# Kernel optimization log

Hardware: AMD Instinct MI355X
Metric: run time of the kernel (lower is better)

The kernel has to match this reference:

```python
import jax, jax.numpy as jnp
import numpy as np

B, N, C, H = 2, 4096, 256, 4
DH = C // H  # 64
EPS = 1e-6
TEMPERATURE = 1.0


def setup_inputs() -> dict:
    key = jax.random.key(0)
    ks = jax.random.split(key, 12)
    s = 0.02
    return {
        "x": jax.random.normal(ks[0], (B, N, C), dtype=jnp.float32),
        "pos_embed": jax.random.normal(ks[1], (B, N, C), dtype=jnp.float32),
        # per-head Q/K/V linear weights stacked over heads (torch Linear(dim, dim_head))
        "Wq": jax.random.normal(ks[2], (H, C, DH), dtype=jnp.float32) * s,
        "bq": jax.random.normal(ks[3], (H, DH), dtype=jnp.float32) * s,
        "Wk": jax.random.normal(ks[4], (H, C, DH), dtype=jnp.float32) * s,
        "bk": jax.random.normal(ks[5], (H, DH), dtype=jnp.float32) * s,
        "Wv": jax.random.normal(ks[6], (H, C, DH), dtype=jnp.float32) * s,
        "bv": jax.random.normal(ks[7], (H, DH), dtype=jnp.float32) * s,
        "Wo": jax.random.normal(ks[8], (C, C), dtype=jnp.float32) * s,
        "bo": jax.random.normal(ks[9], (C,), dtype=jnp.float32) * s,
        "ln_g": jnp.ones((C,), dtype=jnp.float32),
        "ln_b": jnp.zeros((C,), dtype=jnp.float32),
    }


def reference(x, pos_embed, Wq, bq, Wk, bk, Wv, bv, Wo, bo, ln_g, ln_b):
    dk = TEMPERATURE * jnp.sqrt(jnp.float32(DH))
    # pre-norm: x + pos_embed -> dropout(p=0, identity) -> LayerNorm(eps=1e-6)
    h = x + pos_embed
    mu = jnp.mean(h, axis=-1, keepdims=True)
    var = jnp.mean(jnp.square(h - mu), axis=-1, keepdims=True)
    h = (h - mu) * jax.lax.rsqrt(var + EPS) * ln_g + ln_b  # [B,N,C]
    # all heads at once (original loops over heads with separate small Linears)
    q = jnp.einsum("bnc,hcd->bhnd", h, Wq) + bq[None, :, None, :]
    k = jnp.einsum("bnc,hcd->bhnd", h, Wk) + bk[None, :, None, :]
    v = jnp.einsum("bnc,hcd->bhnd", h, Wv) + bv[None, :, None, :]
    scores = jnp.einsum("bhid,bhjd->bhij", q, k) / dk  # [B,H,N,N]
    # NOTE: original uses F.softmax(dot_prod, dim=1) on [B,N,N] -> normalize over
    # the QUERY axis i, not the key axis j. Replicated faithfully here (axis=2).
    attn = jax.nn.softmax(scores, axis=2)
    o = jnp.einsum("bhij,bhjd->bhid", attn, v)  # [B,H,N,DH]
    o = jnp.transpose(o, (0, 2, 1, 3)).reshape(B, N, C)  # concat heads on channel
    return o @ Wo + bo
```

## Files before the change

### kernel.cpp

```cpp
#include <hip/hip_runtime.h>
#include <math.h>

#define B_ 2
#define N_ 4096
#define C_ 256
#define H_ 4
#define DH_ 64
#define EPS_ 1e-6f
#define SCALE_Q_ 0.18033688011112042f

typedef short bf16x8 __attribute__((ext_vector_type(8)));
typedef short bf16x4v __attribute__((ext_vector_type(4)));
typedef float f32x4 __attribute__((ext_vector_type(4)));
typedef int i32x4 __attribute__((ext_vector_type(4)));

#define MFMA32(a, b, c) __builtin_amdgcn_mfma_f32_16x16x32_bf16(a, b, c, 0, 0, 0)
#define FAST_EXP2(x) __builtin_amdgcn_exp2f(x)

__device__ __forceinline__ unsigned short f2bf(float x) {
  unsigned int u = __float_as_uint(x);
  return (unsigned short)((u + 0x7FFFu + ((u >> 16) & 1u)) >> 16);
}
__device__ __forceinline__ float bf2f(unsigned short u) {
  return __uint_as_float(((unsigned int)u) << 16);
}
__device__ __forceinline__ int pack2bf(float lo, float hi) {
  return (int)__builtin_amdgcn_perm(__float_as_uint(hi) + 0x8000u,
                                    __float_as_uint(lo) + 0x8000u, 0x07060302u);
}

__global__ __launch_bounds__(256) void ln_kernel(
    const float* __restrict__ x, const float* __restrict__ pos,
    const float* __restrict__ g, const float* __restrict__ beta,
    unsigned short* __restrict__ h16) {
  const int w = threadIdx.x >> 6, lane = threadIdx.x & 63;
  const int row = blockIdx.x * 4 + w;
  const float4 xv = *(const float4*)&x[row * C_ + lane * 4];
  const float4 pv = *(const float4*)&pos[row * C_ + lane * 4];
  float4 v = {xv.x + pv.x, xv.y + pv.y, xv.z + pv.z, xv.w + pv.w};
  float s = v.x + v.y + v.z + v.w;
  s += __shfl_xor(s, 1);  s += __shfl_xor(s, 2);  s += __shfl_xor(s, 4);
  s += __shfl_xor(s, 8);  s += __shfl_xor(s, 16); s += __shfl_xor(s, 32);
  const float mu = s * (1.0f / C_);
  float4 d = {v.x - mu, v.y - mu, v.z - mu, v.w - mu};
  float q = d.x * d.x + d.y * d.y + d.z * d.z + d.w * d.w;
  q += __shfl_xor(q, 1);  q += __shfl_xor(q, 2);  q += __shfl_xor(q, 4);
  q += __shfl_xor(q, 8);  q += __shfl_xor(q, 16); q += __shfl_xor(q, 32);
  const float rs = rsqrtf(q * (1.0f / C_) + EPS_);
  const float4 g4 = *(const float4*)&g[lane * 4];
  const float4 b4 = *(const float4*)&beta[lane * 4];
  bf16x4v o;
  o[0] = (short)f2bf(d.x * rs * g4.x + b4.x);
  o[1] = (short)f2bf(d.y * rs * g4.y + b4.y);
  o[2] = (short)f2bf(d.z * rs * g4.z + b4.z);
  o[3] = (short)f2bf(d.w * rs * g4.w + b4.w);
  *(bf16x4v*)&h16[row * C_ + lane * 4] = o;
}

__global__ __launch_bounds__(256) void wconv_kernel(
    const float* __restrict__ Wq, const float* __restrict__ Wk,
    const float* __restrict__ Wv, const float* __restrict__ Wo,
    unsigned short* __restrict__ W3T, unsigned short* __restrict__ WoT) {
  const int base = blockIdx.x * 2048;
#pragma unroll
  for (int p = 0; p < 8; p++) {
    const int idx = base + p * 256 + threadIdx.x;
    if (idx < 196608) {
      const int m = idx >> 14;
      const int rem = idx & 16383;
      const int c = rem >> 6, d = rem & 63;
      const int h = m / 3, kind = m - h * 3;
      const float* W = kind == 0 ? Wq : kind == 1 ? Wk : Wv;
      float v = W[h * 16384 + rem];
      if (kind == 0) v *= SCALE_Q_;
      W3T[(h * 192 + kind * 64 + d) * 256 + c] = f2bf(v);
    } else {
      const int widx = idx - 196608;
      const int k = widx >> 8, n = widx & 255;
      WoT[n * 256 + k] = f2bf(Wo[widx]);
    }
  }
}

__global__ __launch_bounds__(256) void qkv_kernel(
    const unsigned short* __restrict__ h16, const unsigned short* __restrict__ W3T,
    const float* __restrict__ bq, const float* __restrict__ bk,
    const float* __restrict__ bv,
    unsigned short* __restrict__ q16, unsigned short* __restrict__ k16,
    unsigned short* __restrict__ vT16) {
  const int rt = blockIdx.x;
  const int hh = blockIdx.y;
  const int t = threadIdx.x;
  const int w = t >> 6, lane = t & 63, c = lane & 15, quad = lane >> 4;
  __shared__ unsigned short Hs[64 * 64];
  __shared__ unsigned short Bs[192 * 64];
  const int row0 = rt * 64;

  f32x4 acc[12];
#pragma unroll
  for (int nt = 0; nt < 12; nt++) acc[nt] = (f32x4){0.f, 0.f, 0.f, 0.f};

  for (int kt = 0; kt < C_; kt += 64) {
    __syncthreads();
#pragma unroll
    for (int p = 0; p < 2; p++) {
      const int e = t + p * 256;
      const int row = e >> 3, ch = e & 7;
      *(bf16x8*)&Hs[row * 64 + ((ch ^ (row & 7)) * 8)] =
          *(const bf16x8*)&h16[(size_t)(row0 + row) * C_ + kt + ch * 8];
    }
#pragma unroll
    for (int p = 0; p < 6; p++) {
      const int e = t + p * 256;
      const int row = e >> 3, ch = e & 7;
      *(bf16x8*)&Bs[row * 64 + ((ch ^ (row & 7)) * 8)] =
          *(const bf16x8*)&W3T[(size_t)(hh * 192 + row) * C_ + kt + ch * 8];
    }
    __syncthreads();
#pragma unroll
    for (int kh = 0; kh < 2; kh++) {
      const int i = w * 16 + c;
      bf16x8 a = *(const bf16x8*)&Hs[i * 64 + (((kh * 4 + quad) ^ (i & 7)) * 8)];
#pragma unroll
      for (int nt = 0; nt < 12; nt++) {
        const int n = nt * 16 + c;
        bf16x8 b = *(const bf16x8*)&Bs[n * 64 + (((kh * 4 + quad) ^ (n & 7)) * 8)];
        acc[nt] = MFMA32(a, b, acc[nt]);
      }
    }
  }
#pragma unroll
  for (int nt = 0; nt < 12; nt++) {
    const int kind = nt >> 2;
    const int col = (nt & 3) * 16 + c;
    const float bias = kind == 0 ? bq[hh * 64 + col] * SCALE_Q_
                     : kind == 1 ? bk[hh * 64 + col] : bv[hh * 64 + col];
#pragma unroll
    for (int r = 0; r < 4; r++) {
      const int gr = row0 + w * 16 + quad * 4 + r;
      const int b = gr >> 12, n = gr & (N_ - 1);
      const size_t bh = (size_t)(b * H_ + hh);
      const unsigned short val = f2bf(acc[nt][r] + bias);
      if (kind == 0)      q16[(bh * N_ + n) * DH_ + col] = val;
      else if (kind == 1) k16[(bh * N_ + n) * DH_ + col] = val;
      else                vT16[(bh * DH_ + col) * N_ + n] = val;
    }
  }
}

__global__ __launch_bounds__(256, 4) void colstats_kernel(
    const unsigned short* __restrict__ q16, const unsigned short* __restrict__ k16,
    unsigned short* __restrict__ vT16) {
  const int blk = blockIdx.x;
  const int bh = blk & 7;
  const int j0 = (blk >> 3) * 32;
  const int t = threadIdx.x;
  const int w = t >> 6, lane = t & 63, c = lane & 15, quad = lane >> 4;
  __shared__ float Lp[4][32];
  __shared__ float ilv[32];

  bf16x8 ka[2][2];
#pragma unroll
  for (int jb = 0; jb < 2; jb++) {
    const size_t kb = ((size_t)bh * N_ + j0 + jb * 16 + c) * DH_;
    ka[jb][0] = *(const bf16x8*)&k16[kb + quad * 8];
    ka[jb][1] = *(const bf16x8*)&k16[kb + 32 + quad * 8];
  }

  f32x4 lsum[2];
#pragma unroll
  for (int jb = 0; jb < 2; jb++) lsum[jb] = (f32x4){0.f, 0.f, 0.f, 0.f};

  for (int i0 = 0; i0 < N_; i0 += 256) {
#pragma unroll
    for (int is = 0; is < 4; is++) {
      const size_t qb = ((size_t)bh * N_ + i0 + w * 64 + is * 16 + c) * DH_;
      bf16x8 qf0 = *(const bf16x8*)&q16[qb + quad * 8];
      bf16x8 qf1 = *(const bf16x8*)&q16[qb + 32 + quad * 8];
#pragma unroll
      for (int jb = 0; jb < 2; jb++) {
        f32x4 s = {0.f, 0.f, 0.f, 0.f};
        s = MFMA32(ka[jb][0], qf0, s);
        s = MFMA32(ka[jb][1], qf1, s);
#pragma unroll
        for (int r = 0; r < 4; r++) lsum[jb][r] += FAST_EXP2(s[r]);
      }
    }
  }
#pragma unroll
  for (int jb = 0; jb < 2; jb++) {
#pragma unroll
    for (int r = 0; r < 4; r++) {
      float s = lsum[jb][r];
      s += __shfl_xor(s, 1); s += __shfl_xor(s, 2);
      s += __shfl_xor(s, 4); s += __shfl_xor(s, 8);
      if (c == 0) Lp[w][jb * 16 + quad * 4 + r] = s;
    }
  }
  __syncthreads();
  if (t < 32) ilv[t] = 1.0f / (Lp[0][t] + Lp[1][t] + Lp[2][t] + Lp[3][t]);
  __syncthreads();
  {
    const int d = t >> 2, ch = t & 3;
    const size_t addr = ((size_t)bh * DH_ + d) * N_ + j0 + ch * 8;
    bf16x8 v = *(const bf16x8*)&vT16[addr];
#pragma unroll
    for (int jj = 0; jj < 8; jj++)
      v[jj] = (short)f2bf(bf2f((unsigned short)v[jj]) * ilv[ch * 8 + jj]);
    *(bf16x8*)&vT16[addr] = v;
  }
}

__global__ __launch_bounds__(512, 4) void attnout_kernel(
    const unsigned short* __restrict__ q16, const unsigned short* __restrict__ k16,
    const unsigned short* __restrict__ vT16, unsigned short* __restrict__ ob16) {
  const int blk = blockIdx.x;
  const int bh = blk & 7;
  const int bb = bh >> 2, hh = bh & 3;
  const int i0 = (blk >> 3) * 64;
  const int t = threadIdx.x;
  const int w = t >> 6, lane = t & 63, c = lane & 15, quad = lane >> 4;
  const int iw = w >> 2;
  const int jw = w & 3;

  __shared__ __align__(16) char smem[32768];
  unsigned short* Ks = (unsigned short*)smem;
  unsigned short* Vs = (unsigned short*)smem + 128 * 64;
  float* Rf = (float*)smem;

  bf16x8 qa[2][2];
#pragma unroll
  for (int ib = 0; ib < 2; ib++) {
    const size_t qb = ((size_t)bh * N_ + i0 + iw * 32 + ib * 16 + c) * DH_;
    qa[ib][0] = *(const bf16x8*)&q16[qb + quad * 8];
    qa[ib][1] = *(const bf16x8*)&q16[qb + 32 + quad * 8];
  }

  bf16x8 kpre[2], vpre[2];
  auto loadKV = [&](int jt) {
#pragma unroll
    for (int p = 0; p < 2; p++) {
      const int e = t + p * 512;
      kpre[p] = *(const bf16x8*)&k16[((size_t)bh * N_ + jt + (e >> 3)) * DH_ + (e & 7) * 8];
      vpre[p] = *(const bf16x8*)&vT16[((size_t)bh * DH_ + (e >> 4)) * N_ + jt + (e & 15) * 8];
    }
  };
  loadKV(0);

  f32x4 of[2][4];
#pragma unroll
  for (int ib = 0; ib < 2; ib++)
#pragma unroll
    for (int dt = 0; dt < 4; dt++) of[ib][dt] = (f32x4){0.f, 0.f, 0.f, 0.f};

  for (int jt = 0; jt < N_; jt += 128) {
    __syncthreads();
#pragma unroll
    for (int p = 0; p < 2; p++) {
      const int e = t + p * 512;
      { const int row = e >> 3, ch = e & 7;
        *(bf16x8*)&Ks[row * 64 + ((ch ^ ((row >> 2) & 7)) * 8)] = kpre[p]; }
      { const int d = e >> 4, ch = e & 15;
        *(bf16x8*)&Vs[d * 128 + ((ch ^ (d & 15)) * 8)] = vpre[p]; }
    }
    __syncthreads();
    if (jt + 128 < N_) loadKV(jt + 128);

    bf16x8 kf[2][2];
#pragma unroll
    for (int s = 0; s < 2; s++) {
      const int jr = jw * 32 + ((c >> 2) * 8) + s * 4 + (c & 3);
      const int swz = (jr >> 2) & 7;
      kf[s][0] = *(const bf16x8*)&Ks[jr * 64 + ((quad ^ swz) * 8)];
      kf[s][1] = *(const bf16x8*)&Ks[jr * 64 + (((4 + quad) ^ swz) * 8)];
    }
    bf16x8 vf[4];
#pragma unroll
    for (int dt = 0; dt < 4; dt++) {
      const int d = dt * 16 + c;
      vf[dt] = *(const bf16x8*)&Vs[d * 128 + (((jw * 4 + quad) ^ (d & 15)) * 8)];
    }

#pragma unroll
    for (int ib = 0; ib < 2; ib++) {
      f32x4 s0 = {0.f, 0.f, 0.f, 0.f}, s1 = {0.f, 0.f, 0.f, 0.f};
      s0 = MFMA32(kf[0][0], qa[ib][0], s0);
      s0 = MFMA32(kf[0][1], qa[ib][1], s0);
      s1 = MFMA32(kf[1][0], qa[ib][0], s1);
      s1 = MFMA32(kf[1][1], qa[ib][1], s1);
      i32x4 pi;
      pi[0] = pack2bf(FAST_EXP2(s0[0]), FAST_EXP2(s0[1]));
      pi[1] = pack2bf(FAST_EXP2(s0[2]), FAST_EXP2(s0[3]));
      pi[2] = pack2bf(FAST_EXP2(s1[0]), FAST_EXP2(s1[1]));
      pi[3] = pack2bf(FAST_EXP2(s1[2]), FAST_EXP2(s1[3]));
      bf16x8 pf = *(bf16x8*)&pi;
#pragma unroll
      for (int dt = 0; dt < 4; dt++)
        of[ib][dt] = MFMA32(pf, vf[dt], of[ib][dt]);
    }
  }

  __syncthreads();
  if (jw >= 2) {
    float* dst = Rf + (iw * 2 + (jw - 2)) * 2048;
#pragma unroll
    for (int ib = 0; ib < 2; ib++)
#pragma unroll
      for (int dt = 0; dt < 4; dt++)
        *(f32x4*)&dst[lane * 32 + (((ib * 4 + dt) ^ (lane & 7)) * 4)] = of[ib][dt];
  }
  __syncthreads();
  if (jw < 2) {
    const float* src = Rf + (iw * 2 + jw) * 2048;
#pragma unroll
    for (int ib = 0; ib < 2; ib++)
#pragma unroll
      for (int dt = 0; dt < 4; dt++)
        of[ib][dt] += *(const f32x4*)&src[lane * 32 + (((ib * 4 + dt) ^ (lane & 7)) * 4)];
  }
  __syncthreads();
  if (jw == 1) {
    float* dst = Rf + iw * 2048;
#pragma unroll
    for (int ib = 0; ib < 2; ib++)
#pragma unroll
      for (int dt = 0; dt < 4; dt++)
        *(f32x4*)&dst[lane * 32 + (((ib * 4 + dt) ^ (lane & 7)) * 4)] = of[ib][dt];
  }
  __syncthreads();
  if (jw == 0) {
    const float* src = Rf + iw * 2048;
#pragma unroll
    for (int ib = 0; ib < 2; ib++)
#pragma unroll
      for (int dt = 0; dt < 4; dt++) {
        of[ib][dt] += *(const f32x4*)&src[lane * 32 + (((ib * 4 + dt) ^ (lane & 7)) * 4)];
#pragma unroll
        for (int r = 0; r < 4; r++)
          ob16[((size_t)bb * N_ + i0 + iw * 32 + ib * 16 + quad * 4 + r) * C_ +
               hh * DH_ + dt * 16 + c] = f2bf(of[ib][dt][r]);
      }
  }
}

__global__ __launch_bounds__(256) void outproj_kernel(
    const unsigned short* __restrict__ ob16, const unsigned short* __restrict__ WoT,
    const float* __restrict__ bo, float* __restrict__ out) {
  const int rt = blockIdx.x;
  const int t = threadIdx.x;
  const int w = t >> 6, lane = t & 63, c = lane & 15, quad = lane >> 4;
  __shared__ unsigned short As[32 * 64];
  __shared__ unsigned short Bs[256 * 64];

  f32x4 acc[2][4];
#pragma unroll
  for (int mt = 0; mt < 2; mt++)
#pragma unroll
    for (int nt = 0; nt < 4; nt++) acc[mt][nt] = (f32x4){0.f, 0.f, 0.f, 0.f};

  for (int kt = 0; kt < C_; kt += 64) {
    __syncthreads();
    {
      const int row = t >> 3, ch = t & 7;
      *(bf16x8*)&As[row * 64 + ((ch ^ (row & 7)) * 8)] =
          *(const bf16x8*)&ob16[((size_t)rt * 32 + row) * C_ + kt + ch * 8];
    }
#pragma unroll
    for (int p = 0; p < 8; p++) {
      const int e = t + p * 256;
      const int row = e >> 3, ch = e & 7;
      *(bf16x8*)&Bs[row * 64 + ((ch ^ (row & 7)) * 8)] =
          *(const bf16x8*)&WoT[(size_t)row * C_ + kt + ch * 8];
    }
    __syncthreads();
#pragma unroll
    for (int kh = 0; kh < 2; kh++) {
      bf16x8 a[2];
#pragma unroll
      for (int mt = 0; mt < 2; mt++) {
        const int i = mt * 16 + c;
        a[mt] = *(const bf16x8*)&As[i * 64 + (((kh * 4 + quad) ^ (i & 7)) * 8)];
      }
#pragma unroll
      for (int nt = 0; nt < 4; nt++) {
        const int n = w * 64 + nt * 16 + c;
        bf16x8 b = *(const bf16x8*)&Bs[n * 64 + (((kh * 4 + quad) ^ (n & 7)) * 8)];
        acc[0][nt] = MFMA32(a[0], b, acc[0][nt]);
        acc[1][nt] = MFMA32(a[1], b, acc[1][nt]);
      }
    }
  }
#pragma unroll
  for (int mt = 0; mt < 2; mt++)
#pragma unroll
    for (int nt = 0; nt < 4; nt++) {
      const int col = w * 64 + nt * 16 + c;
      const float bias = bo[col];
#pragma unroll
      for (int r = 0; r < 4; r++)
        out[((size_t)rt * 32 + mt * 16 + quad * 4 + r) * C_ + col] = acc[mt][nt][r] + bias;
    }
}

extern "C" void kernel_launch(void* const* d_in, const int* in_sizes, int n_in,
                              void* d_out, int out_size, void* d_ws, size_t ws_size,
                              hipStream_t stream) {
  const float* x    = (const float*)d_in[0];
  const float* pos  = (const float*)d_in[1];
  const float* Wq   = (const float*)d_in[2];
  const float* bq   = (const float*)d_in[3];
  const float* Wk   = (const float*)d_in[4];
  const float* bk   = (const float*)d_in[5];
  const float* Wv   = (const float*)d_in[6];
  const float* bv   = (const float*)d_in[7];
  const float* Wo   = (const float*)d_in[8];
  const float* bo   = (const float*)d_in[9];
  const float* ln_g = (const float*)d_in[10];
  const float* ln_b = (const float*)d_in[11];
  float* out = (float*)d_out;

  const size_t SZ = (size_t)B_ * N_ * C_;
  unsigned short* h16  = (unsigned short*)d_ws;
  unsigned short* q16  = h16 + SZ;
  unsigned short* k16  = q16 + SZ;
  unsigned short* vT16 = k16 + SZ;
  unsigned short* ob16 = vT16 + SZ;
  unsigned short* W3T  = ob16 + SZ;
  unsigned short* WoT  = W3T + (size_t)H_ * 192 * 256;

  ln_kernel<<<B_ * N_ / 4, 256, 0, stream>>>(x, pos, ln_g, ln_b, h16);
  wconv_kernel<<<128, 256, 0, stream>>>(Wq, Wk, Wv, Wo, W3T, WoT);
  qkv_kernel<<<dim3(128, H_), 256, 0, stream>>>(h16, W3T, bq, bk, bv, q16, k16, vT16);
  colstats_kernel<<<1024, 256, 0, stream>>>(q16, k16, vT16);
  attnout_kernel<<<512, 512, 0, stream>>>(q16, k16, vT16, ob16);
  outproj_kernel<<<256, 256, 0, stream>>>(ob16, WoT, bo, out);
}
```

Before: 213.0 us.

## Stage Q tiles in swizzled LDS with prefetch and widen colstats key block

The column-statistics kernel now handles 64 keys per block with 512 threads instead of 32 keys with 256. Each 128-row Q tile is loaded cooperatively from global memory into XOR-swizzled shared memory, and the next tile is prefetched into registers while the current one is computed. The aim is to halve redundant global Q reads across blocks and to hide load latency. In exchange it adds two barriers per tile and more LDS and register pressure, and the grid shrinks to 512 blocks.

New measurement: 471.8 us. 122% more time.

```diff
diff --git a/kernel.cpp b/kernel.cpp
--- a/kernel.cpp
+++ b/kernel.cpp
@@ -148,47 +148,65 @@
   }
 }
 
-__global__ __launch_bounds__(256, 4) void colstats_kernel(
+__global__ __launch_bounds__(512, 4) void colstats_kernel(
     const unsigned short* __restrict__ q16, const unsigned short* __restrict__ k16,
     unsigned short* __restrict__ vT16) {
   const int blk = blockIdx.x;
   const int bh = blk & 7;
-  const int j0 = (blk >> 3) * 32;
+  const int j0 = (blk >> 3) * 64;
   const int t = threadIdx.x;
   const int w = t >> 6, lane = t & 63, c = lane & 15, quad = lane >> 4;
-  __shared__ float Lp[4][32];
-  __shared__ float ilv[32];
-
-  bf16x8 ka[2][2];
-#pragma unroll
-  for (int jb = 0; jb < 2; jb++) {
+  __shared__ unsigned short Qs[128 * 64];
+  __shared__ float Lp[8][64];
+  __shared__ float ilv[64];
+
+  bf16x8 ka[4][2];
+#pragma unroll
+  for (int jb = 0; jb < 4; jb++) {
     const size_t kb = ((size_t)bh * N_ + j0 + jb * 16 + c) * DH_;
     ka[jb][0] = *(const bf16x8*)&k16[kb + quad * 8];
     ka[jb][1] = *(const bf16x8*)&k16[kb + 32 + quad * 8];
   }
 
-  f32x4 lsum[2];
-#pragma unroll
-  for (int jb = 0; jb < 2; jb++) lsum[jb] = (f32x4){0.f, 0.f, 0.f, 0.f};
-
-  for (int i0 = 0; i0 < N_; i0 += 256) {
-#pragma unroll
-    for (int is = 0; is < 4; is++) {
-      const size_t qb = ((size_t)bh * N_ + i0 + w * 64 + is * 16 + c) * DH_;
-      bf16x8 qf0 = *(const bf16x8*)&q16[qb + quad * 8];
-      bf16x8 qf1 = *(const bf16x8*)&q16[qb + 32 + quad * 8];
-#pragma unroll
-      for (int jb = 0; jb < 2; jb++) {
-        f32x4 s = {0.f, 0.f, 0.f, 0.f};
-        s = MFMA32(ka[jb][0], qf0, s);
-        s = MFMA32(ka[jb][1], qf1, s);
-#pragma unroll
-        for (int r = 0; r < 4; r++) lsum[jb][r] += FAST_EXP2(s[r]);
-      }
-    }
-  }
-#pragma unroll
-  for (int jb = 0; jb < 2; jb++) {
+  bf16x8 pre[2];
+  auto loadQ = [&](int i0) {
+#pragma unroll
+    for (int p = 0; p < 2; p++) {
+      const int e = t + p * 512;
+      const int row = e >> 3, ch = e & 7;
+      pre[p] = *(const bf16x8*)&q16[((size_t)bh * N_ + i0 + row) * DH_ + ch * 8];
+    }
+  };
+  loadQ(0);
+
+  f32x4 lsum[4];
+#pragma unroll
+  for (int jb = 0; jb < 4; jb++) lsum[jb] = (f32x4){0.f, 0.f, 0.f, 0.f};
+
+  for (int i0 = 0; i0 < N_; i0 += 128) {
+    __syncthreads();
+#pragma unroll
+    for (int p = 0; p < 2; p++) {
+      const int e = t + p * 512;
+      const int row = e >> 3, ch = e & 7;
+      *(bf16x8*)&Qs[row * 64 + ((ch ^ (row & 7)) * 8)] = pre[p];
+    }
+    __syncthreads();
+    if (i0 + 128 < N_) loadQ(i0 + 128);
+    const int ir = w * 16 + c;
+    bf16x8 qf0 = *(const bf16x8*)&Qs[ir * 64 + ((quad ^ (c & 7)) * 8)];
+    bf16x8 qf1 = *(const bf16x8*)&Qs[ir * 64 + (((4 + quad) ^ (c & 7)) * 8)];
+#pragma unroll
+    for (int jb = 0; jb < 4; jb++) {
+      f32x4 s = {0.f, 0.f, 0.f, 0.f};
+      s = MFMA32(ka[jb][0], qf0, s);
+      s = MFMA32(ka[jb][1], qf1, s);
+#pragma unroll
+      for (int r = 0; r < 4; r++) lsum[jb][r] += FAST_EXP2(s[r]);
+    }
+  }
+#pragma unroll
+  for (int jb = 0; jb < 4; jb++) {
 #pragma unroll
     for (int r = 0; r < 4; r++) {
       float s = lsum[jb][r];
@@ -198,10 +216,15 @@
     }
   }
   __syncthreads();
-  if (t < 32) ilv[t] = 1.0f / (Lp[0][t] + Lp[1][t] + Lp[2][t] + Lp[3][t]);
+  if (t < 64) {
+    float l = 0.f;
+#pragma unroll
+    for (int ww = 0; ww < 8; ww++) l += Lp[ww][t];
+    ilv[t] = 1.0f / l;
+  }
   __syncthreads();
   {
-    const int d = t >> 2, ch = t & 3;
+    const int d = t >> 3, ch = t & 7;
     const size_t addr = ((size_t)bh * DH_ + d) * N_ + j0 + ch * 8;
     bf16x8 v = *(const bf16x8*)&vT16[addr];
 #pragma unroll
@@ -431,7 +454,7 @@
   ln_kernel<<<B_ * N_ / 4, 256, 0, stream>>>(x, pos, ln_g, ln_b, h16);
   wconv_kernel<<<128, 256, 0, stream>>>(Wq, Wk, Wv, Wo, W3T, WoT);
   qkv_kernel<<<dim3(128, H_), 256, 0, stream>>>(h16, W3T, bq, bk, bv, q16, k16, vT16);
-  colstats_kernel<<<1024, 256, 0, stream>>>(q16, k16, vT16);
+  colstats_kernel<<<512, 512, 0, stream>>>(q16, k16, vT16);
   attnout_kernel<<<512, 512, 0, stream>>>(q16, k16, vT16, ob16);
   outproj_kernel<<<256, 256, 0, stream>>>(ob16, WoT, bo, out);
 }
```
